# Optimization experiments

Hardware: AMD Instinct MI355X
Metric: run time of the kernel (lower is better)

## Reference

```python
import jax, jax.numpy as jnp
import numpy as np

NBASE = 4                       # number of bases (DNA)
NSTATE = 2 * NBASE * (NBASE + 1)  # = 40 flip-flop transition states
SCALE = 5.0
LARGE_LOG_VAL = 50000.0


def setup_inputs() -> dict:
    key = jax.random.key(0)
    kx, kw, kb = jax.random.split(key, 3)
    T, N, INSIZE = 2048, 128, 256
    x = jax.random.normal(kx, (T, N, INSIZE), dtype=jnp.float32)
    # orthonormal-ish init approximated by scaled gaussian
    W = jax.random.normal(kw, (NSTATE, INSIZE), dtype=jnp.float32) / np.float32(np.sqrt(INSIZE))
    b = 0.5 * jax.random.normal(kb, (NSTATE,), dtype=jnp.float32)
    return {"x": x, "W": W, "b": b}


def _log_partition_flipflop(scores):
    """Forward-algorithm log partition function. scores: (T, N, C)."""
    T, N, C = scores.shape
    fwd0 = jnp.concatenate(
        [jnp.zeros((N, NBASE), scores.dtype),
         jnp.full((N, NBASE), -LARGE_LOG_VAL, scores.dtype)], axis=1)
    logZ0 = jax.nn.logsumexp(fwd0, axis=1, keepdims=True)  # (N, 1)
    fwd0 = fwd0 - logZ0

    def step(carry, scores_t):
        fwd, logZ = carry
        # (N, nbase+1, 2*nbase): to-state grouped transition scores
        curr = fwd[:, None, :] + scores_t.reshape(N, NBASE + 1, 2 * NBASE)
        base1 = jax.nn.logsumexp(curr[:, :NBASE], axis=2)            # (N, nbase) flip states
        base2 = jnp.logaddexp(curr[:, NBASE, :NBASE],
                              curr[:, NBASE, NBASE:])               # (N, nbase) flop states
        new_state = jnp.concatenate([base1, base2], axis=1)          # (N, 2*nbase)
        factors = jax.nn.logsumexp(new_state, axis=1, keepdims=True)  # (N, 1)
        return (new_state - factors, logZ + factors), None

    (_, logZ), _ = jax.lax.scan(step, (fwd0, logZ0), scores)
    return logZ  # (N, 1)


def reference(x, W, b):
    T = x.shape[0]
    # scale * tanh(x W^T + b) -> transition scores (T, N, NSTATE)
    y = SCALE * jnp.tanh(jnp.einsum('tni,ci->tnc', x, W) + b)
    logZ = _log_partition_flipflop(y)          # (N, 1)
    return y - logZ / np.float32(T)            # broadcast over T and C
```

## Files before the change

### kernel.cpp

```cpp
#include <hip/hip_runtime.h>
#include <hip/hip_bf16.h>

#define T_DIM 2048
#define N_DIM 128
#define K_DIM 256
#define C_DIM 40
#define SEG 256
#define SEGLEN 8
#define GRP 8
#define SEGPERGRP 32

typedef __attribute__((ext_vector_type(8))) short bf16x8;
typedef __attribute__((ext_vector_type(4))) float f32x4v;

__device__ __forceinline__ unsigned pack_bf16(float a, float b) {
    union { float f; unsigned u; } ua, ub;
    ua.f = a; ub.f = b;
    unsigned ra = (ua.u + 0x7FFFu + ((ua.u >> 16) & 1u)) >> 16;
    unsigned rb = (ub.u + 0x7FFFu + ((ub.u >> 16) & 1u)) >> 16;
    return (ra & 0xFFFFu) | (rb << 16);
}

__device__ __forceinline__ unsigned cvt_pk(float a, float b) {
    unsigned r;
    asm("v_cvt_pk_bf16_f32 %0, %1, %2" : "=v"(r) : "v"(a), "v"(b));
    return r;
}

__device__ __forceinline__ float bf_lo(unsigned u) {
    union { unsigned x; float f; } v; v.x = u << 16; return v.f;
}
__device__ __forceinline__ float bf_hi(unsigned u) {
    union { unsigned x; float f; } v; v.x = u & 0xFFFF0000u; return v.f;
}

__device__ __forceinline__ float fast_tanh(float v) {
    float e = __expf(2.f * v);
    return 1.f - 2.f / (e + 1.f);
}

__global__ __launch_bounds__(256, 2) void k_gemm_tanh(
    const float* __restrict__ x, const float* __restrict__ W,
    const float* __restrict__ b, unsigned* __restrict__ ybf)
{
    __shared__ __align__(16) float shX[4][2][16][128];

    const int tid = threadIdx.x;
    const int lane = tid & 63;
    const int wave = tid >> 6;
    const int lr = lane & 15;
    const int kg = lane >> 4;
    const int bid = blockIdx.x;
    const int sbid = (bid & 7) * 64 + (bid >> 3);
    const int gw = sbid * 4 + wave;

    bf16x8 wf[3][8];
    #pragma unroll
    for (int cb = 0; cb < 3; ++cb) {
        #pragma unroll
        for (int kk = 0; kk < 8; ++kk) {
            int rowc = cb * 16 + lr;
            float4 w0 = {0.f, 0.f, 0.f, 0.f}, w1 = {0.f, 0.f, 0.f, 0.f};
            if (rowc < C_DIM) {
                const float* wp = W + rowc * K_DIM + kg * 8 + kk * 32;
                w0 = *reinterpret_cast<const float4*>(wp);
                w1 = *reinterpret_cast<const float4*>(wp + 4);
            }
            union { bf16x8 v; unsigned u[4]; } uw;
            uw.u[0] = pack_bf16(w0.x, w0.y);
            uw.u[1] = pack_bf16(w0.z, w0.w);
            uw.u[2] = pack_bf16(w1.x, w1.y);
            uw.u[3] = pack_bf16(w1.z, w1.w);
            wf[cb][kk] = uw.v;
        }
    }

    float4 bia0 = *reinterpret_cast<const float4*>(b + kg * 4);
    float4 bia1 = *reinterpret_cast<const float4*>(b + 16 + kg * 4);
    float4 bia2 = {0.f, 0.f, 0.f, 0.f};
    if (kg < 2) bia2 = *reinterpret_cast<const float4*>(b + 32 + kg * 4);

    auto stage = [&](int h) {
        size_t tile = (size_t)(h >> 1) * 2048 + gw;
        const char* gbase = reinterpret_cast<const char*>(x)
                          + tile * 16384 + (h & 1) * 512;
        float* lbase = &shX[wave][h & 1][0][0];
        #pragma unroll
        for (int j = 0; j < 8; ++j) {
            int r = 2 * j + (lane >> 5);
            const void* gp = gbase + r * 1024 + (lane & 31) * 16;
            __builtin_amdgcn_global_load_lds(
                (const __attribute__((address_space(1))) void*)gp,
                (__attribute__((address_space(3))) void*)(lbase + j * 256),
                16, 0, 0);
        }
    };

    f32x4v acc0, acc1, acc2;

#define COMPUTE_HALF(KH)                                                          \
    do {                                                                          \
        const char* cX = reinterpret_cast<const char*>(&shX[wave][KH][0][0]);     \
        _Pragma("unroll")                                                         \
        for (int kt = 0; kt < 4; ++kt) {                                          \
            int k0 = kg * 32 + kt * 128;                                          \
            float4 d0 = *reinterpret_cast<const float4*>(cX + lr * 512 + k0);      \
            float4 d1 = *reinterpret_cast<const float4*>(cX + lr * 512 + k0 + 16); \
            union { bf16x8 v; unsigned u[4]; } xf;                                \
            xf.u[0] = cvt_pk(d0.x, d0.y);                                         \
            xf.u[1] = cvt_pk(d0.z, d0.w);                                         \
            xf.u[2] = cvt_pk(d1.x, d1.y);                                         \
            xf.u[3] = cvt_pk(d1.z, d1.w);                                         \
            acc0 = __builtin_amdgcn_mfma_f32_16x16x32_bf16(wf[0][KH * 4 + kt], xf.v, acc0, 0, 0, 0); \
            acc1 = __builtin_amdgcn_mfma_f32_16x16x32_bf16(wf[1][KH * 4 + kt], xf.v, acc1, 0, 0, 0); \
            acc2 = __builtin_amdgcn_mfma_f32_16x16x32_bf16(wf[2][KH * 4 + kt], xf.v, acc2, 0, 0, 0); \
        }                                                                         \
    } while (0)

    stage(0);
    stage(1);

    for (int t = 0; t < 8; ++t) {
        __builtin_amdgcn_sched_barrier(0);
        if (t == 0) asm volatile("s_waitcnt vmcnt(8)" ::: "memory");
        else        asm volatile("s_waitcnt vmcnt(11)" ::: "memory");
        __builtin_amdgcn_sched_barrier(0);
        acc0 = (f32x4v){0.f, 0.f, 0.f, 0.f};
        acc1 = (f32x4v){0.f, 0.f, 0.f, 0.f};
        acc2 = (f32x4v){0.f, 0.f, 0.f, 0.f};
        COMPUTE_HALF(0);
        __builtin_amdgcn_sched_barrier(0);
        if (t < 7) stage(2 * t + 2);

        __builtin_amdgcn_sched_barrier(0);
        if (t < 7) asm volatile("s_waitcnt vmcnt(8)" ::: "memory");
        else       asm volatile("s_waitcnt vmcnt(0)" ::: "memory");
        __builtin_amdgcn_sched_barrier(0);
        COMPUTE_HALF(1);

        size_t row = ((size_t)t * 2048 + gw) * 16 + lr;
        unsigned* yr = ybf + row * 20;
        float o00 = 5.f * fast_tanh(acc0[0] + bia0.x);
        float o01 = 5.f * fast_tanh(acc0[1] + bia0.y);
        float o02 = 5.f * fast_tanh(acc0[2] + bia0.z);
        float o03 = 5.f * fast_tanh(acc0[3] + bia0.w);
        float o10 = 5.f * fast_tanh(acc1[0] + bia1.x);
        float o11 = 5.f * fast_tanh(acc1[1] + bia1.y);
        float o12 = 5.f * fast_tanh(acc1[2] + bia1.z);
        float o13 = 5.f * fast_tanh(acc1[3] + bia1.w);
        uint2 p0, p1;
        p0.x = cvt_pk(o00, o01); p0.y = cvt_pk(o02, o03);
        p1.x = cvt_pk(o10, o11); p1.y = cvt_pk(o12, o13);
        *reinterpret_cast<uint2*>(yr + kg * 2) = p0;
        *reinterpret_cast<uint2*>(yr + 8 + kg * 2) = p1;
        if (kg < 2) {
            float o20 = 5.f * fast_tanh(acc2[0] + bia2.x);
            float o21 = 5.f * fast_tanh(acc2[1] + bia2.y);
            float o22 = 5.f * fast_tanh(acc2[2] + bia2.z);
            float o23 = 5.f * fast_tanh(acc2[3] + bia2.w);
            uint2 p2;
            p2.x = cvt_pk(o20, o21); p2.y = cvt_pk(o22, o23);
            *reinterpret_cast<uint2*>(yr + 16 + kg * 2) = p2;
        }

        __builtin_amdgcn_sched_barrier(0);
        if (t < 7) stage(2 * t + 3);
    }
#undef COMPUTE_HALF
}

__global__ __launch_bounds__(128) void k_seg(
    const unsigned* __restrict__ ybf, float* __restrict__ segv, float* __restrict__ segl)
{
    int tid = blockIdx.x * 128 + threadIdx.x;
    int n = tid & 127;
    int s = tid >> 7;

    float P[8][8];
    #pragma unroll
    for (int j = 0; j < 8; ++j)
        #pragma unroll
        for (int c = 0; c < 8; ++c) P[j][c] = (j == c) ? 1.f : 0.f;

    for (int st = 0; st < SEGLEN; ++st) {
        int t = s * SEGLEN + st;
        const unsigned* yr = ybf + ((size_t)t * N_DIM + n) * 20;
        float e[40];
        #pragma unroll
        for (int i = 0; i < 5; ++i) {
            uint4 w = reinterpret_cast<const uint4*>(yr)[i];
            e[i * 8 + 0] = __expf(bf_lo(w.x));
            e[i * 8 + 1] = __expf(bf_hi(w.x));
            e[i * 8 + 2] = __expf(bf_lo(w.y));
            e[i * 8 + 3] = __expf(bf_hi(w.y));
            e[i * 8 + 4] = __expf(bf_lo(w.z));
            e[i * 8 + 5] = __expf(bf_hi(w.z));
            e[i * 8 + 6] = __expf(bf_lo(w.w));
            e[i * 8 + 7] = __expf(bf_hi(w.w));
        }
        #pragma unroll
        for (int c = 0; c < 8; ++c) {
            float np[8];
            #pragma unroll
            for (int j = 0; j < 4; ++j) {
                float a = 0.f;
                #pragma unroll
                for (int i = 0; i < 8; ++i) a += P[i][c] * e[j * 8 + i];
                np[j] = a;
            }
            #pragma unroll
            for (int j = 0; j < 4; ++j)
                np[4 + j] = P[j][c] * e[32 + j] + P[4 + j][c] * e[36 + j];
            #pragma unroll
            for (int j = 0; j < 8; ++j) P[j][c] = np[j];
        }
    }
    #pragma unroll
    for (int c = 0; c < 8; ++c) {
        float sum = 0.f;
        #pragma unroll
        for (int j = 0; j < 8; ++j) sum += P[j][c];
        float inv = 1.f / sum;
        #pragma unroll
        for (int j = 0; j < 8; ++j)
            segv[(((size_t)s * 8 + c) * 8 + j) * N_DIM + n] = P[j][c] * inv;
        segl[((size_t)s * 8 + c) * N_DIM + n] = __logf(sum);
    }
}

__global__ __launch_bounds__(128) void k_grp(
    const float* __restrict__ segv, const float* __restrict__ segl,
    float* __restrict__ grpv, float* __restrict__ grpl)
{
    int tid = blockIdx.x * 128 + threadIdx.x;
    int n = tid & 127;
    int cc = (tid >> 7) & 7;
    int g = tid >> 10;

    float u[8];
    #pragma unroll
    for (int i = 0; i < 8; ++i) u[i] = (i == cc) ? 1.f : 0.f;
    float logacc = 0.f;

    for (int s = g * SEGPERGRP; s < (g + 1) * SEGPERGRP; ++s) {
        float l[8];
        #pragma unroll
        for (int i = 0; i < 8; ++i) l[i] = segl[((size_t)s * 8 + i) * N_DIM + n];
        float m = l[0];
        #pragma unroll
        for (int i = 1; i < 8; ++i) m = fmaxf(m, l[i]);
        float nu[8] = {0.f, 0.f, 0.f, 0.f, 0.f, 0.f, 0.f, 0.f};
        #pragma unroll
        for (int i = 0; i < 8; ++i) {
            float wi = u[i] * __expf(l[i] - m);
            #pragma unroll
            for (int j = 0; j < 8; ++j)
                nu[j] += wi * segv[(((size_t)s * 8 + i) * 8 + j) * N_DIM + n];
        }
        float sum = 0.f;
        #pragma unroll
        for (int j = 0; j < 8; ++j) sum += nu[j];
        float inv = 1.f / sum;
        #pragma unroll
        for (int j = 0; j < 8; ++j) u[j] = nu[j] * inv;
        logacc += m + __logf(sum);
    }
    #pragma unroll
    for (int j = 0; j < 8; ++j)
        grpv[(((size_t)g * 8 + cc) * 8 + j) * N_DIM + n] = u[j];
    grpl[((size_t)g * 8 + cc) * N_DIM + n] = logacc;
}

__global__ void k_fin(const float* __restrict__ grpv, const float* __restrict__ grpl,
                      float* __restrict__ lz)
{
    int n = threadIdx.x;
    float p[8] = {0.25f, 0.25f, 0.25f, 0.25f, 0.f, 0.f, 0.f, 0.f};
    float logZ = 1.3862943611198906f;

    for (int g = 0; g < GRP; ++g) {
        float l[8];
        #pragma unroll
        for (int i = 0; i < 8; ++i) l[i] = grpl[((size_t)g * 8 + i) * N_DIM + n];
        float m = l[0];
        #pragma unroll
        for (int i = 1; i < 8; ++i) m = fmaxf(m, l[i]);
        float nu[8] = {0.f, 0.f, 0.f, 0.f, 0.f, 0.f, 0.f, 0.f};
        #pragma unroll
        for (int i = 0; i < 8; ++i) {
            float wi = p[i] * __expf(l[i] - m);
            #pragma unroll
            for (int j = 0; j < 8; ++j)
                nu[j] += wi * grpv[(((size_t)g * 8 + i) * 8 + j) * N_DIM + n];
        }
        float sum = 0.f;
        #pragma unroll
        for (int j = 0; j < 8; ++j) sum += nu[j];
        float inv = 1.f / sum;
        #pragma unroll
        for (int j = 0; j < 8; ++j) p[j] = nu[j] * inv;
        logZ += m + __logf(sum);
    }
    lz[n] = logZ * (1.f / (float)T_DIM);
}

__global__ __launch_bounds__(256) void k_sub(const unsigned* __restrict__ ybf,
                                             const float* __restrict__ lz,
                                             float* __restrict__ out)
{
    int i = blockIdx.x * 256 + threadIdx.x;
    int n = (i / 10) & 127;
    float d = lz[n];
    uint2 w = *reinterpret_cast<const uint2*>(ybf + 2 * (size_t)i);
    float4 v;
    v.x = bf_lo(w.x) - d;
    v.y = bf_hi(w.x) - d;
    v.z = bf_lo(w.y) - d;
    v.w = bf_hi(w.y) - d;
    reinterpret_cast<float4*>(out)[i] = v;
}

extern "C" void kernel_launch(void* const* d_in, const int* in_sizes, int n_in,
                              void* d_out, int out_size, void* d_ws, size_t ws_size,
                              hipStream_t stream) {
    const float* x = (const float*)d_in[0];
    const float* W = (const float*)d_in[1];
    const float* b = (const float*)d_in[2];
    float* out = (float*)d_out;
    float* ws = (float*)d_ws;

    unsigned* ybf = (unsigned*)ws;
    float* segv = ws + 5242880;
    float* segl = ws + 7340032;
    float* grpv = ws + 7602176;
    float* grpl = ws + 7667712;
    float* lz   = ws + 7675904;

    k_gemm_tanh<<<512, 256, 0, stream>>>(x, W, b, ybf);
    k_seg<<<256, 128, 0, stream>>>(ybf, segv, segl);
    k_grp<<<64, 128, 0, stream>>>(segv, segl, grpv, grpl);
    k_fin<<<1, 128, 0, stream>>>(grpv, grpl, lz);
    k_sub<<<10240, 256, 0, stream>>>(ybf, lz, out);
}
```

Measured before the change: 142.5 us.

## Replace direct global-to-LDS loads with register-staged, XOR-swizzled LDS pipeline

The GEMM-tanh kernel no longer uses global_load_lds with explicit vmcnt waits. It loads quarter-K tiles into registers, writes them to LDS with an XOR swizzle to avoid bank conflicts, and double-buffers across two smaller LDS buffers, overlapping the next load with the current MFMA compute. This halves LDS usage and removes the hand-tuned waitcnt scheduling. In exchange it uses more VGPRs and leaves load/store ordering to the compiler, with no explicit barriers between the LDS write and read, which relies on each buffer being private to one wave.

```diff
diff --git a/kernel.cpp b/kernel.cpp
--- a/kernel.cpp
+++ b/kernel.cpp
@@ -43,7 +43,7 @@
     const float* __restrict__ x, const float* __restrict__ W,
     const float* __restrict__ b, unsigned* __restrict__ ybf)
 {
-    __shared__ __align__(16) float shX[4][2][16][128];
+    __shared__ __align__(16) float shX[4][2][16][64];
 
     const int tid = threadIdx.x;
     const int lane = tid & 63;
@@ -53,6 +53,9 @@
     const int bid = blockIdx.x;
     const int sbid = (bid & 7) * 64 + (bid >> 3);
     const int gw = sbid * 4 + wave;
+    const int ldr = lane >> 4;
+    const int ldc = (lane & 15) * 16;
+    const int sw = (lr & 7) << 4;
 
     bf16x8 wf[3][8];
     #pragma unroll
@@ -80,65 +83,74 @@
     float4 bia2 = {0.f, 0.f, 0.f, 0.f};
     if (kg < 2) bia2 = *reinterpret_cast<const float4*>(b + 32 + kg * 4);
 
-    auto stage = [&](int h) {
-        size_t tile = (size_t)(h >> 1) * 2048 + gw;
-        const char* gbase = reinterpret_cast<const char*>(x)
-                          + tile * 16384 + (h & 1) * 512;
-        float* lbase = &shX[wave][h & 1][0][0];
-        #pragma unroll
-        for (int j = 0; j < 8; ++j) {
-            int r = 2 * j + (lane >> 5);
-            const void* gp = gbase + r * 1024 + (lane & 31) * 16;
-            __builtin_amdgcn_global_load_lds(
-                (const __attribute__((address_space(1))) void*)gp,
-                (__attribute__((address_space(3))) void*)(lbase + j * 256),
-                16, 0, 0);
-        }
-    };
-
+    const char* xb = reinterpret_cast<const char*>(x);
+    char* lds0 = reinterpret_cast<char*>(&shX[wave][0][0][0]);
+    char* lds1 = reinterpret_cast<char*>(&shX[wave][1][0][0]);
+
+    float4 rA[4], rB[4];
     f32x4v acc0, acc1, acc2;
 
-#define COMPUTE_HALF(KH)                                                          \
-    do {                                                                          \
-        const char* cX = reinterpret_cast<const char*>(&shX[wave][KH][0][0]);     \
-        _Pragma("unroll")                                                         \
-        for (int kt = 0; kt < 4; ++kt) {                                          \
-            int k0 = kg * 32 + kt * 128;                                          \
-            float4 d0 = *reinterpret_cast<const float4*>(cX + lr * 512 + k0);      \
-            float4 d1 = *reinterpret_cast<const float4*>(cX + lr * 512 + k0 + 16); \
-            union { bf16x8 v; unsigned u[4]; } xf;                                \
-            xf.u[0] = cvt_pk(d0.x, d0.y);                                         \
-            xf.u[1] = cvt_pk(d0.z, d0.w);                                         \
-            xf.u[2] = cvt_pk(d1.x, d1.y);                                         \
-            xf.u[3] = cvt_pk(d1.z, d1.w);                                         \
-            acc0 = __builtin_amdgcn_mfma_f32_16x16x32_bf16(wf[0][KH * 4 + kt], xf.v, acc0, 0, 0, 0); \
-            acc1 = __builtin_amdgcn_mfma_f32_16x16x32_bf16(wf[1][KH * 4 + kt], xf.v, acc1, 0, 0, 0); \
-            acc2 = __builtin_amdgcn_mfma_f32_16x16x32_bf16(wf[2][KH * 4 + kt], xf.v, acc2, 0, 0, 0); \
-        }                                                                         \
+#define LOADP(R, TT, P)                                                        \
+    do {                                                                       \
+        const char* base_ = xb + ((size_t)(TT) * 2048 + gw) * 16384 + (P) * 256; \
+        _Pragma("unroll")                                                      \
+        for (int j = 0; j < 4; ++j)                                            \
+            R[j] = *reinterpret_cast<const float4*>(base_ + (4 * j + ldr) * 1024 + ldc); \
     } while (0)
 
-    stage(0);
-    stage(1);
-
-    for (int t = 0; t < 8; ++t) {
-        __builtin_amdgcn_sched_barrier(0);
-        if (t == 0) asm volatile("s_waitcnt vmcnt(8)" ::: "memory");
-        else        asm volatile("s_waitcnt vmcnt(11)" ::: "memory");
-        __builtin_amdgcn_sched_barrier(0);
+#define WRITEP(R, LB)                                                          \
+    do {                                                                       \
+        _Pragma("unroll")                                                      \
+        for (int j = 0; j < 4; ++j) {                                          \
+            int r_ = 4 * j + ldr;                                              \
+            *reinterpret_cast<float4*>((LB) + r_ * 256 + (ldc ^ ((r_ & 7) << 4))) = R[j]; \
+        }                                                                      \
+    } while (0)
+
+#define COMPUTEP(LB, P)                                                        \
+    do {                                                                       \
+        _Pragma("unroll")                                                      \
+        for (int ks = 0; ks < 2; ++ks) {                                       \
+            int c_ = ks * 128 + kg * 32;                                       \
+            float4 d0 = *reinterpret_cast<const float4*>((LB) + lr * 256 + (c_ ^ sw));        \
+            float4 d1 = *reinterpret_cast<const float4*>((LB) + lr * 256 + ((c_ + 16) ^ sw)); \
+            union { bf16x8 v; unsigned u[4]; } xf;                             \
+            xf.u[0] = cvt_pk(d0.x, d0.y);                                      \
+            xf.u[1] = cvt_pk(d0.z, d0.w);                                      \
+            xf.u[2] = cvt_pk(d1.x, d1.y);                                      \
+            xf.u[3] = cvt_pk(d1.z, d1.w);                                      \
+            acc0 = __builtin_amdgcn_mfma_f32_16x16x32_bf16(wf[0][(P) * 2 + ks], xf.v, acc0, 0, 0, 0); \
+            acc1 = __builtin_amdgcn_mfma_f32_16x16x32_bf16(wf[1][(P) * 2 + ks], xf.v, acc1, 0, 0, 0); \
+            acc2 = __builtin_amdgcn_mfma_f32_16x16x32_bf16(wf[2][(P) * 2 + ks], xf.v, acc2, 0, 0, 0); \
+        }                                                                      \
+    } while (0)
+
+    LOADP(rA, 0, 0);
+    LOADP(rB, 0, 1);
+    WRITEP(rA, lds0);
+
+    for (int tt = 0; tt < 8; ++tt) {
         acc0 = (f32x4v){0.f, 0.f, 0.f, 0.f};
         acc1 = (f32x4v){0.f, 0.f, 0.f, 0.f};
         acc2 = (f32x4v){0.f, 0.f, 0.f, 0.f};
-        COMPUTE_HALF(0);
-        __builtin_amdgcn_sched_barrier(0);
-        if (t < 7) stage(2 * t + 2);
-
-        __builtin_amdgcn_sched_barrier(0);
-        if (t < 7) asm volatile("s_waitcnt vmcnt(8)" ::: "memory");
-        else       asm volatile("s_waitcnt vmcnt(0)" ::: "memory");
-        __builtin_amdgcn_sched_barrier(0);
-        COMPUTE_HALF(1);
-
-        size_t row = ((size_t)t * 2048 + gw) * 16 + lr;
+
+        LOADP(rA, tt, 2);
+        WRITEP(rB, lds1);
+        COMPUTEP(lds0, 0);
+
+        LOADP(rB, tt, 3);
+        WRITEP(rA, lds0);
+        COMPUTEP(lds1, 1);
+
+        if (tt < 7) LOADP(rA, tt + 1, 0);
+        WRITEP(rB, lds1);
+        COMPUTEP(lds0, 2);
+
+        if (tt < 7) LOADP(rB, tt + 1, 1);
+        if (tt < 7) WRITEP(rA, lds0);
+        COMPUTEP(lds1, 3);
+
+        size_t row = ((size_t)tt * 2048 + gw) * 16 + lr;
         unsigned* yr = ybf + row * 20;
         float o00 = 5.f * fast_tanh(acc0[0] + bia0.x);
         float o01 = 5.f * fast_tanh(acc0[1] + bia0.y);
@@ -162,11 +174,10 @@
             p2.x = cvt_pk(o20, o21); p2.y = cvt_pk(o22, o23);
             *reinterpret_cast<uint2*>(yr + 16 + kg * 2) = p2;
         }
-
-        __builtin_amdgcn_sched_barrier(0);
-        if (t < 7) stage(2 * t + 3);
-    }
-#undef COMPUTE_HALF
+    }
+#undef LOADP
+#undef WRITEP
+#undef COMPUTEP
 }
 
 __global__ __launch_bounds__(128) void k_seg(
```

Measured after the change: 152.2 us. 1.07x slower.
